# Kernel tuning notes

Measured on AMD Instinct MI355X. Metric: run time of the kernel, lower is better.

## Reference

```python
import jax, jax.numpy as jnp
import numpy as np

T, DIM, H = 1024, 2048, 16
QLR, KVLR = 1024, 512
NOPE, ROPE, VD = 128, 64, 128
QKD = NOPE + ROPE          # 192
IH, ID, TOPK = 16, 128, 256
EPS = 1e-6

def rmsnorm(x, w):
    return x * jax.lax.rsqrt(jnp.mean(x * x, axis=-1, keepdims=True) + EPS) * w

def layernorm(x, w, b, eps=1e-5):
    m = jnp.mean(x, axis=-1, keepdims=True)
    v = jnp.mean((x - m) ** 2, axis=-1, keepdims=True)
    return (x - m) * jax.lax.rsqrt(v + eps) * w + b

def apply_rope(x, cos, sin):
    # non-interleaved: first half = real, second half = imag
    d = x.shape[-1] // 2
    while cos.ndim < x.ndim:
        cos, sin = cos[:, None], sin[:, None]
    x1, x2 = x[..., :d], x[..., d:]
    return jnp.concatenate([x1 * cos - x2 * sin, x1 * sin + x2 * cos], axis=-1)

def hadamard(x):
    # unnormalized Walsh-Hadamard on last dim (power of 2)
    n = x.shape[-1]
    shape = x.shape
    y, h = x, 1
    while h < n:
        y = y.reshape(shape[:-1] + (-1, 2 * h))
        a, b = y[..., :h], y[..., h:]
        y = jnp.concatenate([a + b, a - b], axis=-1)
        h *= 2
    return y.reshape(shape)

def rotate_activation(x):
    # half-swap then Hadamard on each half
    d = x.shape[-1] // 2
    x1, x2 = x[..., :d], x[..., d:]
    return jnp.concatenate([hadamard(x2), hadamard(x1)], axis=-1)

def setup_inputs() -> dict:
    key = jax.random.key(0)
    ks = jax.random.split(key, 10)
    s = 0.02
    w = lambda k, shp: jax.random.normal(k, shp, jnp.float32) * s
    pos = jnp.arange(T, dtype=jnp.float32)
    inv = 1.0 / (10000.0 ** (jnp.arange(0, ROPE, 2, dtype=jnp.float32) / ROPE))
    ang = pos[:, None] * inv[None, :]
    return {
        'hidden_states': jax.random.normal(ks[0], (T, DIM), jnp.float32),
        'rope_cos': jnp.cos(ang), 'rope_sin': jnp.sin(ang),
        'wq_a': w(ks[1], (QLR, DIM)),
        'q_norm_w': jnp.ones((QLR,), jnp.float32),
        'wq_b': w(ks[2], (H * QKD, QLR)),
        'wkv_a': w(ks[3], (KVLR + ROPE, DIM)),
        'kv_norm_w': jnp.ones((KVLR,), jnp.float32),
        'wkv_b': w(ks[4], (H * (NOPE + VD), KVLR)),
        'wo': w(ks[5], (DIM, H * VD)),
        'iq_norm_w': jnp.ones((QLR,), jnp.float32),
        'iwq_b': w(ks[6], (IH * ID, QLR)),
        'iwk': w(ks[7], (IH * ID, DIM)),
        'k_norm_w': jnp.ones((ID,), jnp.float32),
        'k_norm_b': jnp.zeros((ID,), jnp.float32),
        'wproj': w(ks[8], (IH, DIM)),
    }

def reference(hidden_states, rope_cos, rope_sin, wq_a, q_norm_w, wq_b,
              wkv_a, kv_norm_w, wkv_b, wo, iq_norm_w, iwq_b, iwk,
              k_norm_w, k_norm_b, wproj):
    x = hidden_states
    t = x.shape[0]
    qr = x @ wq_a.T                                   # [t, QLR]

    # ---- lightning indexer: top-k causal token selection ----
    iq = (rmsnorm(qr, iq_norm_w) @ iwq_b.T).reshape(t, IH, ID)
    iq = jnp.concatenate([apply_rope(iq[..., :ROPE], rope_cos, rope_sin), iq[..., ROPE:]], -1)
    iq = rotate_activation(iq)
    ik = layernorm((x @ iwk.T).reshape(t, IH, ID), k_norm_w, k_norm_b)
    ik = jnp.concatenate([apply_rope(ik[..., :ROPE], rope_cos, rope_sin), ik[..., ROPE:]], -1)
    ik = rotate_activation(ik)
    w = (x @ wproj.T) * (IH ** -0.5) * (ID ** -0.5)   # [t, IH]
    dots = jax.nn.relu(jnp.einsum('thd,shd->ths', iq, ik)) * w[:, :, None]
    score = dots.sum(axis=1)                          # [t, t]
    rows = jnp.arange(t)
    score = jnp.where(rows[None, :] <= rows[:, None], score, -jnp.inf)
    _, topk_idx = jax.lax.top_k(score, TOPK)          # [t, TOPK]
    valid = topk_idx <= rows[:, None]
    safe_idx = jnp.where(valid, topk_idx, 0)

    # ---- MLA latent projections ----
    q = (rmsnorm(qr, q_norm_w) @ wq_b.T).reshape(t, H, QKD)
    q_nope, q_pe = q[..., :NOPE], q[..., NOPE:]
    q_pe = apply_rope(q_pe, rope_cos, rope_sin)
    kv_a = x @ wkv_a.T                                # [t, KVLR+ROPE]
    kv = rmsnorm(kv_a[:, :KVLR], kv_norm_w)
    k_pe = apply_rope(kv_a[:, KVLR:], rope_cos, rope_sin)
    wkv = wkv_b.reshape(H, NOPE + VD, KVLR)
    w_k, w_v = wkv[:, :NOPE, :], wkv[:, NOPE:, :]
    q_nope_proj = jnp.einsum('thd,hdc->thc', q_nope, w_k)
    q_key = jnp.concatenate([q_nope_proj, q_pe], -1)  # [t, H, KVLR+ROPE]
    kv_key = jnp.concatenate([kv, k_pe], -1)          # [t, KVLR+ROPE]

    # ---- sparse attention over selected indices ----
    sel = kv_key[safe_idx]                            # [t, TOPK, KVLR+ROPE]
    scale = QKD ** -0.5
    logits = jnp.einsum('thc,tkc->thk', q_key, sel) * scale
    logits = jnp.where(valid[:, None, :], logits, -jnp.inf)
    attn = jax.nn.softmax(logits, axis=-1)
    out_latent = jnp.einsum('thk,tkc->thc', attn, sel[..., :KVLR])
    out_v = jnp.einsum('thc,hdc->thd', out_latent, w_v)
    return out_v.reshape(t, H * VD) @ wo.T            # [t, DIM]
```

## Files before the change

### kernel.cpp

```cpp
#include <hip/hip_runtime.h>
#include <hip/hip_bf16.h>
#include <math.h>

#define T_     1024
#define DIM_   2048
#define H_     16
#define QLR_   1024
#define KVLR_  512
#define NOPE_  128
#define ROPE_  64
#define VD_    128
#define QKD_   192
#define IH_    16
#define ID_    128
#define TOPK_  256
#define CKV_   576

#define SCALE_W    0.022097086912079608f
#define SCALE_LOG  0.07216878364870323f

typedef short bfrag __attribute__((ext_vector_type(8)));
typedef float ffrag __attribute__((ext_vector_type(4)));

__device__ __forceinline__ unsigned short f2bf(float f) {
    union { __hip_bfloat16 h; unsigned short u; } c; c.h = __float2bfloat16(f); return c.u;
}
__device__ __forceinline__ float bf2f(unsigned short u) {
    union { unsigned short u; __hip_bfloat16 h; } c; c.u = u; return __bfloat162float(c.h);
}

__global__ __launch_bounds__(256) void cast_hl_k(
    const float* __restrict__ in, unsigned short* __restrict__ hi,
    unsigned short* __restrict__ lo, long n,
    const float* __restrict__ colw, const float* __restrict__ rowscale, int Kc)
{
    long base = ((long)blockIdx.x * 256 + threadIdx.x) * 4;
    if (base >= n) return;
    float4 v = *(const float4*)(in + base);
    float s[4] = {v.x, v.y, v.z, v.w};
    if (colw) {
        int col = (int)(base % Kc);
        float4 cw = *(const float4*)(colw + col);
        s[0] *= cw.x; s[1] *= cw.y; s[2] *= cw.z; s[3] *= cw.w;
    }
    if (rowscale) {
        float r = rowscale[base / Kc];
        s[0] *= r; s[1] *= r; s[2] *= r; s[3] *= r;
    }
    ushort4 h4;
    h4.x = f2bf(s[0]); h4.y = f2bf(s[1]); h4.z = f2bf(s[2]); h4.w = f2bf(s[3]);
    *(ushort4*)(hi + base) = h4;
    if (lo) {
        ushort4 l4;
        l4.x = f2bf(s[0] - bf2f(h4.x));
        l4.y = f2bf(s[1] - bf2f(h4.y));
        l4.z = f2bf(s[2] - bf2f(h4.z));
        l4.w = f2bf(s[3] - bf2f(h4.w));
        *(ushort4*)(lo + base) = l4;
    }
}

__global__ __launch_bounds__(256) void tcast_k(const float* __restrict__ in,
                                               unsigned short* __restrict__ out)
{
    int h = blockIdx.z, c0 = blockIdx.x * 32, d0 = blockIdx.y * 32;
    __shared__ float t[32][33];
    int tx = threadIdx.x & 31, ty = threadIdx.x >> 5;
    #pragma unroll
    for (int i = 0; i < 4; ++i)
        t[ty + i * 8][tx] = in[(long)(h * 256 + d0 + ty + i * 8) * 512 + c0 + tx];
    __syncthreads();
    #pragma unroll
    for (int i = 0; i < 4; ++i)
        out[((long)h * 512 + c0 + ty + i * 8) * 128 + d0 + tx] = f2bf(t[tx][ty + i * 8]);
}

__global__ __launch_bounds__(256) void gemm_bt_mfma_k(
    const unsigned short* __restrict__ A, const unsigned short* __restrict__ B,
    float* __restrict__ C, long sA, long sB, long sC,
    int lda, int ldb, int ldc, int N, int K)
{
    A += (long)blockIdx.z * sA;
    B += (long)blockIdx.z * sB;
    C += (long)blockIdx.z * sC;
    __shared__ unsigned short As[128 * 40];
    __shared__ unsigned short Bs[128 * 40];
    const int tid = threadIdx.x;
    const int bm = blockIdx.y * 128, bn = blockIdx.x * 128;
    const int wave = tid >> 6, lane = tid & 63;
    const int wm = (wave >> 1) * 64, wn = (wave & 1) * 64;
    const int lm = lane & 15, quad = lane >> 4;

    ffrag acc[4][4];
    #pragma unroll
    for (int mi = 0; mi < 4; ++mi)
        #pragma unroll
        for (int ni = 0; ni < 4; ++ni)
            #pragma unroll
            for (int r = 0; r < 4; ++r) acc[mi][ni][r] = 0.f;

    const int srow = tid >> 1, shalf = tid & 1;
    const long aoff = (long)(bm + srow) * lda + shalf * 16;
    int brow = bn + srow; if (brow > N - 1) brow = N - 1;
    const long boff = (long)brow * ldb + shalf * 16;
    unsigned short* la = As + srow * 40 + shalf * 16;
    unsigned short* lb = Bs + srow * 40 + shalf * 16;

    uint4 va0 = *(const uint4*)(A + aoff);
    uint4 va1 = *(const uint4*)(A + aoff + 8);
    uint4 vb0 = *(const uint4*)(B + boff);
    uint4 vb1 = *(const uint4*)(B + boff + 8);

    for (int k0 = 0; k0 < K; k0 += 32) {
        __syncthreads();
        *(uint4*)la = va0; *(uint4*)(la + 8) = va1;
        *(uint4*)lb = vb0; *(uint4*)(lb + 8) = vb1;
        __syncthreads();
        if (k0 + 32 < K) {
            va0 = *(const uint4*)(A + aoff + k0 + 32);
            va1 = *(const uint4*)(A + aoff + k0 + 40);
            vb0 = *(const uint4*)(B + boff + k0 + 32);
            vb1 = *(const uint4*)(B + boff + k0 + 40);
        }
        bfrag af[4], bf[4];
        #pragma unroll
        for (int mi = 0; mi < 4; ++mi)
            af[mi] = *(const bfrag*)(As + (wm + mi * 16 + lm) * 40 + quad * 8);
        #pragma unroll
        for (int ni = 0; ni < 4; ++ni)
            bf[ni] = *(const bfrag*)(Bs + (wn + ni * 16 + lm) * 40 + quad * 8);
        #pragma unroll
        for (int mi = 0; mi < 4; ++mi)
            #pragma unroll
            for (int ni = 0; ni < 4; ++ni)
                acc[mi][ni] = __builtin_amdgcn_mfma_f32_16x16x32_bf16(
                    af[mi], bf[ni], acc[mi][ni], 0, 0, 0);
    }

    #pragma unroll
    for (int mi = 0; mi < 4; ++mi)
        #pragma unroll
        for (int ni = 0; ni < 4; ++ni) {
            int n = bn + wn + ni * 16 + lm;
            if (n < N) {
                int mb = bm + wm + mi * 16 + quad * 4;
                #pragma unroll
                for (int r = 0; r < 4; ++r)
                    C[(long)(mb + r) * ldc + n] = acc[mi][ni][r];
            }
        }
}

__global__ __launch_bounds__(256) void gemm_bt64_k(
    const unsigned short* __restrict__ A, const unsigned short* __restrict__ B,
    void* __restrict__ Cv, long sA, long sB, long sC,
    int lda, int ldb, int ldc, int N, int K, int obf)
{
    A += (long)blockIdx.z * sA;
    B += (long)blockIdx.z * sB;
    __shared__ unsigned short As[64 * 40];
    __shared__ unsigned short Bs[64 * 40];
    const int tid = threadIdx.x;
    const int bm = blockIdx.y * 64, bn = blockIdx.x * 64;
    const int wave = tid >> 6, lane = tid & 63;
    const int wm = (wave >> 1) * 32, wn = (wave & 1) * 32;
    const int lm = lane & 15, quad = lane >> 4;

    ffrag acc[2][2];
    #pragma unroll
    for (int mi = 0; mi < 2; ++mi)
        #pragma unroll
        for (int ni = 0; ni < 2; ++ni)
            #pragma unroll
            for (int r = 0; r < 4; ++r) acc[mi][ni][r] = 0.f;

    const int srow = tid >> 2, schunk = tid & 3;
    const long aoff = (long)(bm + srow) * lda + schunk * 8;
    int brow = bn + srow; if (brow > N - 1) brow = N - 1;
    const long boff = (long)brow * ldb + schunk * 8;
    unsigned short* la = As + srow * 40 + schunk * 8;
    unsigned short* lb = Bs + srow * 40 + schunk * 8;

    uint4 va = *(const uint4*)(A + aoff);
    uint4 vb = *(const uint4*)(B + boff);

    for (int k0 = 0; k0 < K; k0 += 32) {
        __syncthreads();
        *(uint4*)la = va;
        *(uint4*)lb = vb;
        __syncthreads();
        if (k0 + 32 < K) {
            va = *(const uint4*)(A + aoff + k0 + 32);
            vb = *(const uint4*)(B + boff + k0 + 32);
        }
        bfrag af[2], bf[2];
        #pragma unroll
        for (int mi = 0; mi < 2; ++mi)
            af[mi] = *(const bfrag*)(As + (wm + mi * 16 + lm) * 40 + quad * 8);
        #pragma unroll
        for (int ni = 0; ni < 2; ++ni)
            bf[ni] = *(const bfrag*)(Bs + (wn + ni * 16 + lm) * 40 + quad * 8);
        #pragma unroll
        for (int mi = 0; mi < 2; ++mi)
            #pragma unroll
            for (int ni = 0; ni < 2; ++ni)
                acc[mi][ni] = __builtin_amdgcn_mfma_f32_16x16x32_bf16(
                    af[mi], bf[ni], acc[mi][ni], 0, 0, 0);
    }

    #pragma unroll
    for (int mi = 0; mi < 2; ++mi)
        #pragma unroll
        for (int ni = 0; ni < 2; ++ni) {
            int n = bn + wn + ni * 16 + lm;
            if (n < N) {
                int mb = bm + wm + mi * 16 + quad * 4;
                if (obf) {
                    unsigned short* C = (unsigned short*)Cv + (long)blockIdx.z * sC;
                    #pragma unroll
                    for (int r = 0; r < 4; ++r)
                        C[(long)(mb + r) * ldc + n] = f2bf(acc[mi][ni][r]);
                } else {
                    float* C = (float*)Cv + (long)blockIdx.z * sC;
                    #pragma unroll
                    for (int r = 0; r < 4; ++r)
                        C[(long)(mb + r) * ldc + n] = acc[mi][ni][r];
                }
            }
        }
}

// ... 11 lines not shown

    ffrag acc[2][2];
    #pragma unroll
    for (int mi = 0; mi < 2; ++mi)
        #pragma unroll
        for (int ni = 0; ni < 2; ++ni)
            #pragma unroll
            for (int r = 0; r < 4; ++r) acc[mi][ni][r] = 0.f;

    const int srow = tid >> 2, schunk = tid & 3;
    const long aoff = (long)(bm + srow) * lda + schunk * 8;
    const long boff = (long)(bn + srow) * ldb + schunk * 8;
    const int loff = srow * 40 + schunk * 8;

    uint4 vah = *(const uint4*)(Ah + aoff);
    uint4 val = *(const uint4*)(Al + aoff);
    uint4 vbh = *(const uint4*)(Bh + boff);
    uint4 vbl = *(const uint4*)(Bl + boff);

    for (int k0 = 0; k0 < K; k0 += 32) {
        __syncthreads();
        *(uint4*)(Ahs + loff) = vah;
        *(uint4*)(Als + loff) = val;
        *(uint4*)(Bhs + loff) = vbh;
        *(uint4*)(Bls + loff) = vbl;
        __syncthreads();
        if (k0 + 32 < K) {
            vah = *(const uint4*)(Ah + aoff + k0 + 32);
            val = *(const uint4*)(Al + aoff + k0 + 32);
            vbh = *(const uint4*)(Bh + boff + k0 + 32);
            vbl = *(const uint4*)(Bl + boff + k0 + 32);
        }
        bfrag ah[2], al[2], bh[2], bl[2];
        #pragma unroll
        for (int mi = 0; mi < 2; ++mi) {
            ah[mi] = *(const bfrag*)(Ahs + (wm + mi * 16 + lm) * 40 + quad * 8);
            al[mi] = *(const bfrag*)(Als + (wm + mi * 16 + lm) * 40 + quad * 8);
        }
        #pragma unroll
        for (int ni = 0; ni < 2; ++ni) {
            bh[ni] = *(const bfrag*)(Bhs + (wn + ni * 16 + lm) * 40 + quad * 8);
            bl[ni] = *(const bfrag*)(Bls + (wn + ni * 16 + lm) * 40 + quad * 8);
        }
        #pragma unroll
        for (int mi = 0; mi < 2; ++mi)
            #pragma unroll
            for (int ni = 0; ni < 2; ++ni) {
                acc[mi][ni] = __builtin_amdgcn_mfma_f32_16x16x32_bf16(ah[mi], bh[ni], acc[mi][ni], 0, 0, 0);
                acc[mi][ni] = __builtin_amdgcn_mfma_f32_16x16x32_bf16(ah[mi], bl[ni], acc[mi][ni], 0, 0, 0);
                acc[mi][ni] = __builtin_amdgcn_mfma_f32_16x16x32_bf16(al[mi], bh[ni], acc[mi][ni], 0, 0, 0);
            }
    }

    #pragma unroll
    for (int mi = 0; mi < 2; ++mi)
        #pragma unroll
        for (int ni = 0; ni < 2; ++ni) {
            int n = bn + wn + ni * 16 + lm;
            int mb = bm + wm + mi * 16 + quad * 4;
            #pragma unroll
            for (int r = 0; r < 4; ++r)
                C[(long)(mb + r) * ldc + n] = acc[mi][ni][r];
        }
}

__global__ __launch_bounds__(256) void wtok_k(const float* __restrict__ x,
    const float* __restrict__ wproj, float* __restrict__ wtok)
{
    int t = blockIdx.x, tid = threadIdx.x;
    __shared__ float xs[DIM_];
    for (int c = tid; c < DIM_; c += 256) xs[c] = x[(long)t * DIM_ + c];
    __syncthreads();
    int wave = tid >> 6, lane = tid & 63;
    #pragma unroll
    for (int i = 0; i < 4; ++i) {
        int h = wave * 4 + i;
        float s = 0.f;
        for (int c = lane; c < DIM_; c += 64) s += xs[c] * wproj[(long)h * DIM_ + c];
        for (int off = 32; off; off >>= 1) s += __shfl_xor(s, off, 64);
        if (lane == 0) wtok[(long)t * IH_ + h] = s * SCALE_W;
    }
}

__global__ __launch_bounds__(256) void rstd_k(const float* __restrict__ qr, float* __restrict__ rstd)
{
    int t = blockIdx.x, tid = threadIdx.x;
    float s = 0.f;
    for (int c = tid; c < QLR_; c += 256) { float v = qr[(long)t * QLR_ + c]; s += v * v; }
    __shared__ float red[256];
    red[tid] = s; __syncthreads();
    for (int off = 128; off; off >>= 1) { if (tid < off) red[tid] += red[tid + off]; __syncthreads(); }
    if (tid == 0) rstd[t] = rsqrtf(red[0] / (float)QLR_ + 1e-6f);
}

__device__ __forceinline__ void rope_rotate_128(float* s, float* w2, int tid, int t,
    const float* __restrict__ cosb, const float* __restrict__ sinb)
{
    float n1 = 0.f, n2 = 0.f;
    if (tid < 32) {
        float x1 = s[tid], x2 = s[tid + 32];
        float c = cosb[t * 32 + tid], sn = sinb[t * 32 + tid];
        n1 = x1 * c - x2 * sn;
        n2 = x1 * sn + x2 * c;
    }
    __syncthreads();
    if (tid < 32) { s[tid] = n1; s[tid + 32] = n2; }
    __syncthreads();
    const int g = tid >> 6, p = tid & 63;
    w2[tid] = s[((1 - g) << 6) + p];
    __syncthreads();
    #pragma unroll
    for (int h = 1; h < 64; h <<= 1) {
        float a = w2[tid], b = w2[(g << 6) + (p ^ h)];
        __syncthreads();
        w2[tid] = (p & h) ? (b - a) : (a + b);
        __syncthreads();
    }
}

__global__ __launch_bounds__(128) void transform_iq_k(float* __restrict__ iq,
    const float* __restrict__ cosb, const float* __restrict__ sinb)
{
    int row = blockIdx.x;
    int t = row / IH_;
    int tid = threadIdx.x;
    __shared__ float s[128], w2[128];
    s[tid] = iq[(long)row * 128 + tid];
    __syncthreads();
    rope_rotate_128(s, w2, tid, t, cosb, sinb);
    iq[(long)row * 128 + tid] = w2[tid];
}

__global__ __launch_bounds__(128) void transform_ik_k(float* __restrict__ ik,
    const float* __restrict__ knw, const float* __restrict__ knb,
    const float* __restrict__ cosb, const float* __restrict__ sinb)
{
    int row = blockIdx.x;
    int t = row / IH_;
    int tid = threadIdx.x;
    __shared__ float s[128], w2[128], red[128];
    float v = ik[(long)row * 128 + tid];
    red[tid] = v; __syncthreads();
    for (int off = 64; off; off >>= 1) { if (tid < off) red[tid] += red[tid + off]; __syncthreads(); }
    float m = red[0] / 128.f; __syncthreads();
    float d = v - m;
    red[tid] = d * d; __syncthreads();
    for (int off = 64; off; off >>= 1) { if (tid < off) red[tid] += red[tid + off]; __syncthreads(); }
    float var = red[0] / 128.f;
    s[tid] = d * rsqrtf(var + 1e-5f) * knw[tid] + knb[tid];
    __syncthreads();
    rope_rotate_128(s, w2, tid, t, cosb, sinb);
    ik[(long)row * 128 + tid] = w2[tid];
}

__global__ __launch_bounds__(256) void transform_kv_k(const float* __restrict__ kva,
    float* __restrict__ kvkey, const float* __restrict__ kvnw,
    const float* __restrict__ cosb, const float* __restrict__ sinb)
{
    int t = blockIdx.x, tid = threadIdx.x;
    const float* a = kva + (long)t * CKV_;
    float* o = kvkey + (long)t * CKV_;
    float v0 = a[tid], v1 = a[tid + 256];
    __shared__ float red[256];
    __shared__ float rsh;
    red[tid] = v0 * v0 + v1 * v1; __syncthreads();
    for (int off = 128; off; off >>= 1) { if (tid < off) red[tid] += red[tid + off]; __syncthreads(); }
    if (tid == 0) rsh = rsqrtf(red[0] / (float)KVLR_ + 1e-6f);
    __syncthreads();
    float rs = rsh;
    o[tid]       = v0 * rs * kvnw[tid];
    o[tid + 256] = v1 * rs * kvnw[tid + 256];
    if (tid < 32) {
        float x1 = a[512 + tid], x2 = a[544 + tid];
        float c = cosb[t * 32 + tid], sn = sinb[t * 32 + tid];
        o[512 + tid] = x1 * c - x2 * sn;
        o[544 + tid] = x1 * sn + x2 * c;
    }
}

__global__ __launch_bounds__(64) void qpe_k(const float* __restrict__ q, float* __restrict__ qkey,
    const float* __restrict__ cosb, const float* __restrict__ sinb)
{
    int row = blockIdx.x * 2 + (threadIdx.x >> 5);
    int i = threadIdx.x & 31;
    int t = row / H_;
    const float* qp = q + (long)row * QKD_ + NOPE_;
    float x1 = qp[i], x2 = qp[i + 32];
    float c = cosb[t * 32 + i], sn = sinb[t * 32 + i];
    float* o = qkey + (long)row * CKV_ + 512;
    o[i]      = x1 * c - x2 * sn;
    o[i + 32] = x1 * sn + x2 * c;
}

__global__ __launch_bounds__(256) void score3_k(
    const unsigned short* __restrict__ iqh, const unsigned short* __restrict__ iql,
    const unsigned short* __restrict__ ikh, const unsigned short* __restrict__ ikl,
    const float* __restrict__ wtok, float* __restrict__ score)
{
    const int bt = blockIdx.y, bs = blockIdx.x;
    if (bs > bt) return;
    __shared__ unsigned short Ah[64 * 40], Al[64 * 40], Bh[64 * 40], Bl[64 * 40];
    __shared__ float wts[64][16];
    const int tid = threadIdx.x;
    const int wave = tid >> 6, lane = tid & 63;
    const int wm = (wave >> 1) * 32, wn = (wave & 1) * 32;
    const int lm = lane & 15, quad = lane >> 4;
    const int t0 = bt * 64, s0 = bs * 64;
    const int srow = tid >> 2, schunk = tid & 3;
    const int loff = srow * 40 + schunk * 8;

    for (int e = tid; e < 1024; e += 256)
        wts[e >> 4][e & 15] = wtok[(long)(t0 + (e >> 4)) * IH_ + (e & 15)];

    const long abase = (long)(t0 + srow) * 2048 + schunk * 8;
    const long bbase = (long)(s0 + srow) * 2048 + schunk * 8;

    uint4 pah = *(const uint4*)(iqh + abase);
    uint4 pal = *(const uint4*)(iql + abase);
    uint4 pbh = *(const uint4*)(ikh + bbase);
    uint4 pbl = *(const uint4*)(ikl + bbase);

    float accf[2][2][4] = {};

    for (int h = 0; h < IH_; ++h) {
        ffrag acch[2][2];
        #pragma unroll
        for (int mi = 0; mi < 2; ++mi)
            #pragma unroll
            for (int ni = 0; ni < 2; ++ni)
                #pragma unroll
                for (int r = 0; r < 4; ++r) acch[mi][ni][r] = 0.f;

        #pragma unroll
        for (int k0 = 0; k0 < ID_; k0 += 32) {
            __syncthreads();
            *(uint4*)(Ah + loff) = pah;
            *(uint4*)(Al + loff) = pal;
            *(uint4*)(Bh + loff) = pbh;
            *(uint4*)(Bl + loff) = pbl;
            __syncthreads();
            int step = h * 4 + (k0 >> 5) + 1;
            if (step < 64) {
                int off = (step >> 2) * 128 + (step & 3) * 32;
                pah = *(const uint4*)(iqh + abase + off);
                pal = *(const uint4*)(iql + abase + off);
                pbh = *(const uint4*)(ikh + bbase + off);
                pbl = *(const uint4*)(ikl + bbase + off);
            }
            bfrag ahf[2], alf[2], bhf[2], blf[2];
            #pragma unroll
            for (int mi = 0; mi < 2; ++mi) {
                ahf[mi] = *(const bfrag*)(Ah + (wm + mi * 16 + lm) * 40 + quad * 8);
                alf[mi] = *(const bfrag*)(Al + (wm + mi * 16 + lm) * 40 + quad * 8);
            }
            #pragma unroll
            for (int ni = 0; ni < 2; ++ni) {
                bhf[ni] = *(const bfrag*)(Bh + (wn + ni * 16 + lm) * 40 + quad * 8);
                blf[ni] = *(const bfrag*)(Bl + (wn + ni * 16 + lm) * 40 + quad * 8);
            }
            #pragma unroll
            for (int mi = 0; mi < 2; ++mi)
                #pragma unroll
                for (int ni = 0; ni < 2; ++ni) {
                    acch[mi][ni] = __builtin_amdgcn_mfma_f32_16x16x32_bf16(ahf[mi], bhf[ni], acch[mi][ni], 0, 0, 0);
                    acch[mi][ni] = __builtin_amdgcn_mfma_f32_16x16x32_bf16(ahf[mi], blf[ni], acch[mi][ni], 0, 0, 0);
                    acch[mi][ni] = __builtin_amdgcn_mfma_f32_16x16x32_bf16(alf[mi], bhf[ni], acch[mi][ni], 0, 0, 0);
                }
        }
        #pragma unroll
        for (int mi = 0; mi < 2; ++mi) {
            float wr[4];
            #pragma unroll
            for (int r = 0; r < 4; ++r) wr[r] = wts[wm + mi * 16 + quad * 4 + r][h];
            #pragma unroll
            for (int ni = 0; ni < 2; ++ni)
                #pragma unroll
                for (int r = 0; r < 4; ++r)
                    accf[mi][ni][r] += fmaxf(acch[mi][ni][r], 0.f) * wr[r];
        }
    }
    #pragma unroll
    for (int mi = 0; mi < 2; ++mi)
        #pragma unroll
        for (int ni = 0; ni < 2; ++ni) {
            int s = s0 + wn + ni * 16 + lm;
            int tb = t0 + wm + mi * 16 + quad * 4;
            #pragma unroll
            for (int r = 0; r < 4; ++r)
                score[(long)(tb + r) * T_ + s] = accf[mi][ni][r];
        }
}

__global__ __launch_bounds__(512) void topk_k(const float* __restrict__ score, int* __restrict__ topk)
{
    int t = blockIdx.x, tid = threadIdx.x;
    __shared__ float v[1024];
    __shared__ int ix[1024];
    for (int i = tid; i < 1024; i += 512) {
        v[i] = (i <= t) ? score[(long)t * T_ + i] : -INFINITY;
        ix[i] = i;
    }
    __syncthreads();
    for (int k = 2; k <= 1024; k <<= 1) {
        for (int j = k >> 1; j > 0; j >>= 1) {
            for (int i = tid; i < 1024; i += 512) {
                int l = i ^ j;
                if (l > i) {
                    bool up = ((i & k) == 0);
                    float vi = v[i], vl = v[l];
                    int xi = ix[i], xl = ix[l];
                    bool iBetter = (vi > vl) || (vi == vl && xi < xl);
                    bool doSwap = up ? !iBetter : iBetter;
                    if (doSwap) { v[i] = vl; v[l] = vi; ix[i] = xl; ix[l] = xi; }
                }
            }
            __syncthreads();
        }
    }
    if (tid < 256) topk[(long)t * TOPK_ + tid] = ix[tid];
}

__global__ __launch_bounds__(256, 4) void attn3_k(
    const float* __restrict__ qkey, const unsigned short* __restrict__ kvb,
    const int* __restrict__ topkp, unsigned short* __restrict__ olat)
{
    __shared__ unsigned short U[13568];
    __shared__ float red[16 * 17];
    __shared__ int kidx[256];
    unsigned short* Qbf = U;
    float*          Lg  = (float*)U;
    unsigned short* VT0 = U;
    unsigned short* VT1 = U + 4608;
    unsigned short* Pbf = U + 9344;

    const int t = blockIdx.x, tid = threadIdx.x;
    const int wave = tid >> 6, lane = tid & 63;
    const int lm = lane & 15, quad = lane >> 4;

    kidx[tid] = topkp[(long)t * TOPK_ + tid];
    const float4* q4 = (const float4*)(qkey + (long)t * (H_ * CKV_));
    #pragma unroll
    for (int rep = 0; rep < 9; ++rep) {
        int e4 = rep * 256 + tid;
        float4 v = q4[e4];
        int f = e4 * 4, h = f / CKV_, c = f - h * CKV_;
        ushort4 u4; u4.x = f2bf(v.x); u4.y = f2bf(v.y); u4.z = f2bf(v.z); u4.w = f2bf(v.w);
        *(ushort4*)(Qbf + h * 584 + c) = u4;
    }
    int myk0 = topkp[(long)t * TOPK_ + wave * 64 + 0 * 16 + lm];
    int myk1 = topkp[(long)t * TOPK_ + wave * 64 + 1 * 16 + lm];
    int myk2 = topkp[(long)t * TOPK_ + wave * 64 + 2 * 16 + lm];
    int myk3 = topkp[(long)t * TOPK_ + wave * 64 + 3 * 16 + lm];
    __syncthreads();

    ffrag acc[4];
    #pragma unroll
    for (int ni = 0; ni < 4; ++ni)
        #pragma unroll
        for (int r = 0; r < 4; ++r) acc[ni][r] = 0.f;

    const unsigned short* kb0 = kvb + (long)myk0 * CKV_ + quad * 8;
    const unsigned short* kb1 = kvb + (long)myk1 * CKV_ + quad * 8;
    const unsigned short* kb2 = kvb + (long)myk2 * CKV_ + quad * 8;
    const unsigned short* kb3 = kvb + (long)myk3 * CKV_ + quad * 8;

    bfrag ba[4], bb[4], bc[4];
    #define LDT(DST, C) { \
        DST[0] = *(const bfrag*)(kb0 + (C)); \
        DST[1] = *(const bfrag*)(kb1 + (C)); \
        DST[2] = *(const bfrag*)(kb2 + (C)); \
        DST[3] = *(const bfrag*)(kb3 + (C)); }
    #define PHA_STEP(I, BUF) { \
        bfrag af = *(const bfrag*)(Qbf + lm * 584 + (I) * 32 + quad * 8); \
        _Pragma("unroll") \
        for (int ni = 0; ni < 4; ++ni) \
            acc[ni] = __builtin_amdgcn_mfma_f32_16x16x32_bf16(af, BUF[ni], acc[ni], 0, 0, 0); \
        if ((I) < 15) LDT(BUF, (I) * 32 + 96) }

    LDT(ba, 0) LDT(bb, 32) LDT(bc, 64)
    PHA_STEP(0, ba)  PHA_STEP(1, bb)  PHA_STEP(2, bc)
    PHA_STEP(3, ba)  PHA_STEP(4, bb)  PHA_STEP(5, bc)
    PHA_STEP(6, ba)  PHA_STEP(7, bb)  PHA_STEP(8, bc)
    PHA_STEP(9, ba)  PHA_STEP(10, bb) PHA_STEP(11, bc)
    PHA_STEP(12, ba) PHA_STEP(13, bb) PHA_STEP(14, bc)
    PHA_STEP(15, ba) PHA_STEP(16, bb) PHA_STEP(17, bc)
    #undef PHA_STEP
    #undef LDT

    __syncthreads();
    #pragma unroll
    for (int ni = 0; ni < 4; ++ni)
        #pragma unroll
        for (int r = 0; r < 4; ++r)
            Lg[(quad * 4 + r) * 260 + wave * 64 + ni * 16 + lm] = acc[ni][r];
    __syncthreads();

    {
        int h = tid >> 4, j = tid & 15;
        float m = -INFINITY;
        #pragma unroll
        for (int kk = 0; kk < 16; ++kk) {
            int key = j * 16 + kk;
            if (kidx[key] <= t) m = fmaxf(m, Lg[h * 260 + key]);
        }
        red[h * 17 + j] = m;
        __syncthreads();
        float mh = -INFINITY;
        #pragma unroll
        for (int jj = 0; jj < 16; ++jj) mh = fmaxf(mh, red[h * 17 + jj]);
        __syncthreads();
        float s = 0.f;
        float pv[16];
        #pragma unroll
        for (int kk = 0; kk < 16; ++kk) {
            int key = j * 16 + kk;
            float e = (kidx[key] <= t) ? expf(Lg[h * 260 + key] * SCALE_LOG - mh * SCALE_LOG) : 0.f;
            pv[kk] = e; s += e;
        }
        red[h * 17 + j] = s;
        __syncthreads();
        float sh = 0.f;
        #pragma unroll
        for (int jj = 0; jj < 16; ++jj) sh += red[h * 17 + jj];
        float inv = 1.f / sh;
        #pragma unroll
        for (int kk = 0; kk < 16; ++kk)
            Pbf[h * 264 + j * 16 + kk] = f2bf(pv[kk] * inv);
    }

    const int kpair = tid & 15, cgrp = tid >> 4;
// ... 8 lines not shown
        int ka_ = kidx[((IT) & 7) * 32 + 2 * kpair]; \
        int kb_ = kidx[((IT) & 7) * 32 + 2 * kpair + 1]; \
        long co_ = (long)(((IT) >> 3) * 128 + cgrp * 8); \
        GA = *(const uint4*)(kvb + (long)ka_ * CKV_ + co_); \
        GB = *(const uint4*)(kvb + (long)kb_ * CKV_ + co_); }
    #define STOREB(GA, GB, BUF) { \
        const unsigned short* pa_ = (const unsigned short*)&GA; \
        const unsigned short* pb_ = (const unsigned short*)&GB; \
        _Pragma("unroll") \
        for (int i_ = 0; i_ < 8; ++i_) \
            *(unsigned int*)((BUF) + (cgrp * 8 + i_) * 36 + 2 * kpair) = \
                (unsigned int)pa_[i_] | ((unsigned int)pb_[i_] << 16); }
    #define MFMAB(BUF, IT) { \
        bfrag pa = *(const bfrag*)(Pbf + lm * 264 + ((IT) & 7) * 32 + quad * 8); \
        _Pragma("unroll") \
        for (int ci = 0; ci < 2; ++ci) { \
            int c = wave * 32 + ci * 16 + lm; \
            bfrag bv; \
            ((uint2*)&bv)[0] = *(const uint2*)((BUF) + c * 36 + quad * 8); \
            ((uint2*)&bv)[1] = *(const uint2*)((BUF) + c * 36 + quad * 8 + 4); \
            acc2[ci] = __builtin_amdgcn_mfma_f32_16x16x32_bf16(pa, bv, acc2[ci], 0, 0, 0); } }
    #define OLATST(IT) { \
        int p_ = (IT) >> 3; \
        _Pragma("unroll") \
        for (int ci = 0; ci < 2; ++ci) \
            _Pragma("unroll") \
            for (int r = 0; r < 4; ++r) \
                olat[((long)t * H_ + quad * 4 + r) * 512 + p_ * 128 + wave * 32 + ci * 16 + lm] \
                    = f2bf(acc2[ci][r]); \
        _Pragma("unroll") \
        for (int ci = 0; ci < 2; ++ci) \
            _Pragma("unroll") \
            for (int r = 0; r < 4; ++r) acc2[ci][r] = 0.f; }
    #define LGKBAR() { asm volatile("s_waitcnt lgkmcnt(0)" ::: "memory"); \
                       __builtin_amdgcn_s_barrier(); }

    PREFB(ga0, gb0, 0);
    PREFB(ga1, gb1, 1);
    LGKBAR();
    STOREB(ga0, gb0, VT0);
    LGKBAR();
    for (int it = 0; it < 32; it += 2) {
        STOREB(ga1, gb1, VT1);
        MFMAB(VT0, it);
        if (it + 2 < 32) PREFB(ga0, gb0, it + 2);
        LGKBAR();
        if (it + 2 < 32) STOREB(ga0, gb0, VT0);
        MFMAB(VT1, it + 1);
        if (it + 3 < 32) PREFB(ga1, gb1, it + 3);
        if (((it + 1) & 7) == 7) OLATST(it + 1);
        LGKBAR();
    }
    #undef PREFB
    #undef STOREB
    #undef MFMAB
    #undef OLATST
    #undef LGKBAR
}

extern "C" void kernel_launch(void* const* d_in, const int* in_sizes, int n_in,
                              void* d_out, int out_size, void* d_ws, size_t ws_size,
                              hipStream_t stream)
{
    const float* x          = (const float*)d_in[0];
    const float* cosb       = (const float*)d_in[1];
    const float* sinb       = (const float*)d_in[2];
    const float* wq_a       = (const float*)d_in[3];
    const float* q_norm_w   = (const float*)d_in[4];
    const float* wq_b       = (const float*)d_in[5];
    const float* wkv_a      = (const float*)d_in[6];
    const float* kv_norm_w  = (const float*)d_in[7];
    const float* wkv_b      = (const float*)d_in[8];
    const float* wo         = (const float*)d_in[9];
    const float* iq_norm_w  = (const float*)d_in[10];
    const float* iwq_b      = (const float*)d_in[11];
    const float* iwk        = (const float*)d_in[12];
    const float* k_norm_w   = (const float*)d_in[13];
    const float* k_norm_b   = (const float*)d_in[14];
    const float* wproj      = (const float*)d_in[15];
    float* out = (float*)d_out;

    float* ws    = (float*)d_ws;
    float* qr    = ws;
    float* rstd  = ws + 1048576;
    float* wtok  = ws + 1049600;
    float* kvkey = ws + 1065984;
    int*   topk  = (int*)(ws + 1655808);
    float* qkey  = ws + 1917952;
    float* outv  = ws + 11355136;
    float* U0    = ws + 13452288;
    float* iq    = U0;
    float* ik    = U0 + 2097152;
    float* kva   = U0 + 4194304;
    float* qbuf  = U0 + 4784128;
    float* score = U0 + 7929856;

    unsigned short* qkey_u = (unsigned short*)qkey;
    unsigned short* wqa_hi  = qkey_u;
    unsigned short* wqa_lo  = qkey_u + 2097152;
    unsigned short* iwk_hi  = qkey_u + 4194304;
    unsigned short* iwk_lo  = qkey_u + 8388608;
    unsigned short* iwqb_hi = qkey_u + 12582912;
    unsigned short* iwqb_lo = qkey_u + 14680064;
    unsigned short* qriq_hi = qkey_u + 16777216;
    unsigned short* qriq_lo = qkey_u + 17825792;
    unsigned short* iqbf_hi = qkey_u;
    unsigned short* iqbf_lo = qkey_u + 2097152;
    unsigned short* ikbf_hi = qkey_u + 4194304;
    unsigned short* ikbf_lo = qkey_u + 6291456;
    unsigned short* wkvb_bf = qkey_u + 8388608;
    unsigned short* wo_bf   = qkey_u + 12582912;
    unsigned short* q_u     = (unsigned short*)qbuf;
    unsigned short* x_hi    = q_u;
    unsigned short* x_lo    = q_u + 2097152;
    unsigned short* wkva_hi = q_u + 4194304;
    unsigned short* outv_u  = (unsigned short*)outv;
    unsigned short* wqb_hi  = outv_u;
    unsigned short* qrq_hi  = outv_u + 3145728;
    unsigned short* outv_bf = outv_u;
    unsigned short* qbf     = (unsigned short*)iq;
    unsigned short* wkT     = (unsigned short*)ik;
    unsigned short* kvb     = (unsigned short*)qr;
    unsigned short* olat_bf = (unsigned short*)U0;

    #define CAST(src, hi, lo, n, cw, rs, K) \
        cast_hl_k<<<(n)/1024, 256, 0, stream>>>((src), (hi), (lo), (n), (cw), (rs), (K))

    CAST(x,     x_hi,   x_lo,   2097152L, nullptr, nullptr, 0);
    CAST(wq_a,  wqa_hi, wqa_lo, 2097152L, nullptr, nullptr, 0);
    CAST(iwk,   iwk_hi, iwk_lo, 4194304L, nullptr, nullptr, 0);
    CAST(iwq_b, iwqb_hi,iwqb_lo,2097152L, nullptr, nullptr, 0);
    CAST(wkv_a, wkva_hi,nullptr,1179648L, nullptr, nullptr, 0);
    CAST(wq_b,  wqb_hi, nullptr,3145728L, nullptr, nullptr, 0);

    gemm3_bt64_k<<<dim3(QLR_/64, T_/64), 256, 0, stream>>>(
        x_hi, x_lo, wqa_hi, wqa_lo, qr, DIM_, DIM_, QLR_, DIM_);

    rstd_k<<<T_, 256, 0, stream>>>(qr, rstd);
    CAST(qr, qriq_hi, qriq_lo, 1048576L, iq_norm_w, rstd, QLR_);
    CAST(qr, qrq_hi,  nullptr, 1048576L, q_norm_w,  rstd, QLR_);

    gemm3_bt64_k<<<dim3(IH_*ID_/64, T_/64), 256, 0, stream>>>(
        qriq_hi, qriq_lo, iwqb_hi, iwqb_lo, iq, QLR_, QLR_, IH_*ID_, QLR_);
    gemm3_bt64_k<<<dim3(IH_*ID_/64, T_/64), 256, 0, stream>>>(
        x_hi, x_lo, iwk_hi, iwk_lo, ik, DIM_, DIM_, IH_*ID_, DIM_);

    gemm_bt64_k<<<dim3((CKV_+63)/64, T_/64, 1), 256, 0, stream>>>(
        x_hi, wkva_hi, kva, 0,0,0, DIM_, DIM_, CKV_, CKV_, DIM_, 0);

    gemm_bt64_k<<<dim3(H_*QKD_/64, T_/64, 1), 256, 0, stream>>>(
        qrq_hi, wqb_hi, qbuf, 0,0,0, QLR_, QLR_, H_*QKD_, H_*QKD_, QLR_, 0);

    wtok_k<<<T_, 256, 0, stream>>>(x, wproj, wtok);

    transform_iq_k<<<T_*IH_, 128, 0, stream>>>(iq, cosb, sinb);
    transform_ik_k<<<T_*IH_, 128, 0, stream>>>(ik, k_norm_w, k_norm_b, cosb, sinb);
    transform_kv_k<<<T_, 256, 0, stream>>>(kva, kvkey, kv_norm_w, cosb, sinb);

    CAST(kvkey, kvb, nullptr, 589824L, nullptr, nullptr, 0);

    CAST(iq, iqbf_hi, iqbf_lo, 2097152L, nullptr, nullptr, 0);
    CAST(ik, ikbf_hi, ikbf_lo, 2097152L, nullptr, nullptr, 0);
    score3_k<<<dim3(T_/64, T_/64), 256, 0, stream>>>(iqbf_hi, iqbf_lo, ikbf_hi, ikbf_lo, wtok, score);
    topk_k<<<T_, 512, 0, stream>>>(score, topk);

    CAST(qbuf, qbf, nullptr, 3145728L, nullptr, nullptr, 0);
    tcast_k<<<dim3(16, 4, 16), 256, 0, stream>>>(wkv_b, wkT);
    qpe_k<<<T_*H_/2, 64, 0, stream>>>(qbuf, qkey, cosb, sinb);
    gemm_bt_mfma_k<<<dim3(KVLR_/128, T_/128, H_), 256, 0, stream>>>(
        qbf, wkT, qkey, 192L, 65536L, 576L, H_*QKD_, ID_, H_*CKV_, KVLR_, ID_);

    attn3_k<<<T_, 256, 0, stream>>>(qkey, kvb, topk, olat_bf);

    CAST(wkv_b, wkvb_bf, nullptr, 2097152L, nullptr, nullptr, 0);
    gemm_bt64_k<<<dim3(VD_/64, T_/64, H_), 256, 0, stream>>>(
        olat_bf, wkvb_bf + (long)NOPE_*KVLR_, outv_bf,
        512L, (long)(NOPE_+VD_)*KVLR_, (long)VD_,
        H_*KVLR_, KVLR_, H_*VD_, VD_, KVLR_, 1);

    CAST(wo, wo_bf, nullptr, 4194304L, nullptr, nullptr, 0);
    gemm_bt64_k<<<dim3(DIM_/64, T_/64, 1), 256, 0, stream>>>(
        outv_bf, wo_bf, out, 0,0,0, H_*VD_, H_*VD_, DIM_, DIM_, H_*VD_, 0);

    #undef CAST
    (void)in_sizes; (void)n_in; (void)out_size; (void)ws_size;
}
```

Baseline: 596.0 us.

## Fuse casts and norm/rope transforms, emit bf16 directly, batch weight casts

Merges the six upfront fp32-to-bf16 casts and the two late weight casts into multi-segment cast launches. Fuses the q rmsnorm statistics with both normalized casts, and rewrites the iq/ik/kv transforms with wave-shuffle Hadamard that write bf16 hi/lo outputs directly. The qkey GEMM and qpe now write bf16, so attention loads bf16 queries without converting. This removes several launches and fp32 round trips through memory. It also changes workspace buffer offsets, which risks aliasing between buffers.

```diff
diff --git a/kernel.cpp b/kernel.cpp
--- a/kernel.cpp
+++ b/kernel.cpp
@@ -31,33 +31,81 @@
 
 __global__ __launch_bounds__(256) void cast_hl_k(
     const float* __restrict__ in, unsigned short* __restrict__ hi,
-    unsigned short* __restrict__ lo, long n,
-    const float* __restrict__ colw, const float* __restrict__ rowscale, int Kc)
+    unsigned short* __restrict__ lo, long n)
 {
     long base = ((long)blockIdx.x * 256 + threadIdx.x) * 4;
     if (base >= n) return;
     float4 v = *(const float4*)(in + base);
-    float s[4] = {v.x, v.y, v.z, v.w};
-    if (colw) {
-        int col = (int)(base % Kc);
-        float4 cw = *(const float4*)(colw + col);
-        s[0] *= cw.x; s[1] *= cw.y; s[2] *= cw.z; s[3] *= cw.w;
-    }
-    if (rowscale) {
-        float r = rowscale[base / Kc];
-        s[0] *= r; s[1] *= r; s[2] *= r; s[3] *= r;
-    }
     ushort4 h4;
-    h4.x = f2bf(s[0]); h4.y = f2bf(s[1]); h4.z = f2bf(s[2]); h4.w = f2bf(s[3]);
+    h4.x = f2bf(v.x); h4.y = f2bf(v.y); h4.z = f2bf(v.z); h4.w = f2bf(v.w);
     *(ushort4*)(hi + base) = h4;
     if (lo) {
         ushort4 l4;
-        l4.x = f2bf(s[0] - bf2f(h4.x));
-        l4.y = f2bf(s[1] - bf2f(h4.y));
-        l4.z = f2bf(s[2] - bf2f(h4.z));
-        l4.w = f2bf(s[3] - bf2f(h4.w));
+        l4.x = f2bf(v.x - bf2f(h4.x));
+        l4.y = f2bf(v.y - bf2f(h4.y));
+        l4.z = f2bf(v.z - bf2f(h4.z));
+        l4.w = f2bf(v.w - bf2f(h4.w));
         *(ushort4*)(lo + base) = l4;
     }
+}
+
+struct CastSeg { const float* src; unsigned short* hi; unsigned short* lo; };
+struct CastDesc { CastSeg seg[6]; int bstart[7]; int nseg; };
+
+__global__ __launch_bounds__(256) void castm_k(CastDesc d)
+{
+    int b = blockIdx.x, s = 0;
+    #pragma unroll
+    for (int i = 1; i < 6; ++i) if (i < d.nseg && b >= d.bstart[i]) s = i;
+    long base = ((long)(b - d.bstart[s]) * 256 + threadIdx.x) * 4;
+    float4 v = *(const float4*)(d.seg[s].src + base);
+    ushort4 h4;
+    h4.x = f2bf(v.x); h4.y = f2bf(v.y); h4.z = f2bf(v.z); h4.w = f2bf(v.w);
+    *(ushort4*)(d.seg[s].hi + base) = h4;
+    if (d.seg[s].lo) {
+        ushort4 l4;
+        l4.x = f2bf(v.x - bf2f(h4.x));
+        l4.y = f2bf(v.y - bf2f(h4.y));
+        l4.z = f2bf(v.z - bf2f(h4.z));
+        l4.w = f2bf(v.w - bf2f(h4.w));
+        *(ushort4*)(d.seg[s].lo + base) = l4;
+    }
+}
+
+__global__ __launch_bounds__(256) void qrnorm_k(const float* __restrict__ qr,
+    const float* __restrict__ iqw, const float* __restrict__ qw,
+    unsigned short* __restrict__ qriq_hi, unsigned short* __restrict__ qriq_lo,
+    unsigned short* __restrict__ qrq_hi)
+{
+    int t = blockIdx.x, tid = threadIdx.x;
+    long base = (long)t * QLR_ + tid * 4;
+    float4 v = *(const float4*)(qr + base);
+    __shared__ float red[256];
+    red[tid] = v.x * v.x + v.y * v.y + v.z * v.z + v.w * v.w;
+    __syncthreads();
+    for (int off = 128; off; off >>= 1) { if (tid < off) red[tid] += red[tid + off]; __syncthreads(); }
+    float r = rsqrtf(red[0] / (float)QLR_ + 1e-6f);
+    int col = tid * 4;
+    float4 wi = *(const float4*)(iqw + col);
+    float4 wq = *(const float4*)(qw + col);
+    float s[4] = {v.x, v.y, v.z, v.w};
+    float wiv[4] = {wi.x, wi.y, wi.z, wi.w};
+    float wqv[4] = {wq.x, wq.y, wq.z, wq.w};
+    ushort4 h4, l4, g4;
+    unsigned short* hp = (unsigned short*)&h4;
+    unsigned short* lp = (unsigned short*)&l4;
+    unsigned short* gp = (unsigned short*)&g4;
+    #pragma unroll
+    for (int i = 0; i < 4; ++i) {
+        float ai = s[i] * wiv[i] * r;
+        float aq = s[i] * wqv[i] * r;
+        hp[i] = f2bf(ai);
+        lp[i] = f2bf(ai - bf2f(hp[i]));
+        gp[i] = f2bf(aq);
+    }
+    *(ushort4*)(qriq_hi + base) = h4;
+    *(ushort4*)(qriq_lo + base) = l4;
+    *(ushort4*)(qrq_hi + base) = g4;
 }
 
 __global__ __launch_bounds__(256) void tcast_k(const float* __restrict__ in,
@@ -77,12 +125,11 @@
 
 __global__ __launch_bounds__(256) void gemm_bt_mfma_k(
     const unsigned short* __restrict__ A, const unsigned short* __restrict__ B,
-    float* __restrict__ C, long sA, long sB, long sC,
-    int lda, int ldb, int ldc, int N, int K)
+    void* __restrict__ Cv, long sA, long sB, long sC,
+    int lda, int ldb, int ldc, int N, int K, int obf)
 {
     A += (long)blockIdx.z * sA;
     B += (long)blockIdx.z * sB;
-    C += (long)blockIdx.z * sC;
     __shared__ unsigned short As[128 * 40];
     __shared__ unsigned short Bs[128 * 40];
     const int tid = threadIdx.x;
@@ -144,9 +191,17 @@
             int n = bn + wn + ni * 16 + lm;
             if (n < N) {
                 int mb = bm + wm + mi * 16 + quad * 4;
-                #pragma unroll
-                for (int r = 0; r < 4; ++r)
-                    C[(long)(mb + r) * ldc + n] = acc[mi][ni][r];
+                if (obf) {
+                    unsigned short* C = (unsigned short*)Cv + (long)blockIdx.z * sC;
+                    #pragma unroll
+                    for (int r = 0; r < 4; ++r)
+                        C[(long)(mb + r) * ldc + n] = f2bf(acc[mi][ni][r]);
+                } else {
+                    float* C = (float*)Cv + (long)blockIdx.z * sC;
+                    #pragma unroll
+                    for (int r = 0; r < 4; ++r)
+                        C[(long)(mb + r) * ldc + n] = acc[mi][ni][r];
+                }
             }
         }
 }
@@ -324,84 +379,77 @@
     }
 }
 
-__global__ __launch_bounds__(256) void rstd_k(const float* __restrict__ qr, float* __restrict__ rstd)
-{
-    int t = blockIdx.x, tid = threadIdx.x;
-    float s = 0.f;
-    for (int c = tid; c < QLR_; c += 256) { float v = qr[(long)t * QLR_ + c]; s += v * v; }
-    __shared__ float red[256];
-    red[tid] = s; __syncthreads();
-    for (int off = 128; off; off >>= 1) { if (tid < off) red[tid] += red[tid + off]; __syncthreads(); }
-    if (tid == 0) rstd[t] = rsqrtf(red[0] / (float)QLR_ + 1e-6f);
-}
-
-__device__ __forceinline__ void rope_rotate_128(float* s, float* w2, int tid, int t,
+__global__ __launch_bounds__(256) void transform_iq2_k(const float* __restrict__ iq,
+    unsigned short* __restrict__ hi, unsigned short* __restrict__ lo,
     const float* __restrict__ cosb, const float* __restrict__ sinb)
 {
-    float n1 = 0.f, n2 = 0.f;
-    if (tid < 32) {
-        float x1 = s[tid], x2 = s[tid + 32];
-        float c = cosb[t * 32 + tid], sn = sinb[t * 32 + tid];
-        n1 = x1 * c - x2 * sn;
-        n2 = x1 * sn + x2 * c;
-    }
-    __syncthreads();
-    if (tid < 32) { s[tid] = n1; s[tid + 32] = n2; }
-    __syncthreads();
-    const int g = tid >> 6, p = tid & 63;
-    w2[tid] = s[((1 - g) << 6) + p];
-    __syncthreads();
+    int row = blockIdx.x * 4 + (threadIdx.x >> 6);
+    int p = threadIdx.x & 63;
+    int t = row >> 4;
+    float a = iq[(long)row * 128 + p];
+    float b = iq[(long)row * 128 + 64 + p];
+    float c = cosb[t * 32 + (p & 31)], sn = sinb[t * 32 + (p & 31)];
+    float asw = __shfl_xor(a, 32, 64);
+    a = (p < 32) ? (a * c - asw * sn) : (asw * sn + a * c);
     #pragma unroll
     for (int h = 1; h < 64; h <<= 1) {
-        float a = w2[tid], b = w2[(g << 6) + (p ^ h)];
-        __syncthreads();
-        w2[tid] = (p & h) ? (b - a) : (a + b);
-        __syncthreads();
-    }
-}
-
-__global__ __launch_bounds__(128) void transform_iq_k(float* __restrict__ iq,
-    const float* __restrict__ cosb, const float* __restrict__ sinb)
-{
-    int row = blockIdx.x;
-    int t = row / IH_;
-    int tid = threadIdx.x;
-    __shared__ float s[128], w2[128];
-    s[tid] = iq[(long)row * 128 + tid];
-    __syncthreads();
-    rope_rotate_128(s, w2, tid, t, cosb, sinb);
-    iq[(long)row * 128 + tid] = w2[tid];
-}
-
-__global__ __launch_bounds__(128) void transform_ik_k(float* __restrict__ ik,
+        float a2 = __shfl_xor(a, h, 64);
+        float b2 = __shfl_xor(b, h, 64);
+        a = (p & h) ? (a2 - a) : (a + a2);
+        b = (p & h) ? (b2 - b) : (b + b2);
+    }
+    unsigned short hb = f2bf(b), ha = f2bf(a);
+    hi[(long)row * 128 + p] = hb;
+    hi[(long)row * 128 + 64 + p] = ha;
+    lo[(long)row * 128 + p] = f2bf(b - bf2f(hb));
+    lo[(long)row * 128 + 64 + p] = f2bf(a - bf2f(ha));
+}
+
+__global__ __launch_bounds__(256) void transform_ik2_k(const float* __restrict__ ik,
+    unsigned short* __restrict__ hi, unsigned short* __restrict__ lo,
     const float* __restrict__ knw, const float* __restrict__ knb,
     const float* __restrict__ cosb, const float* __restrict__ sinb)
 {
-    int row = blockIdx.x;
-    int t = row / IH_;
-    int tid = threadIdx.x;
-    __shared__ float s[128], w2[128], red[128];
-    float v = ik[(long)row * 128 + tid];
-    red[tid] = v; __syncthreads();
-    for (int off = 64; off; off >>= 1) { if (tid < off) red[tid] += red[tid + off]; __syncthreads(); }
-    float m = red[0] / 128.f; __syncthreads();
-    float d = v - m;
-    red[tid] = d * d; __syncthreads();
-    for (int off = 64; off; off >>= 1) { if (tid < off) red[tid] += red[tid + off]; __syncthreads(); }
-    float var = red[0] / 128.f;
-    s[tid] = d * rsqrtf(var + 1e-5f) * knw[tid] + knb[tid];
-    __syncthreads();
-    rope_rotate_128(s, w2, tid, t, cosb, sinb);
-    ik[(long)row * 128 + tid] = w2[tid];
-}
-
-__global__ __launch_bounds__(256) void transform_kv_k(const float* __restrict__ kva,
-    float* __restrict__ kvkey, const float* __restrict__ kvnw,
+    int row = blockIdx.x * 4 + (threadIdx.x >> 6);
+    int p = threadIdx.x & 63;
+    int t = row >> 4;
+    float a = ik[(long)row * 128 + p];
+    float b = ik[(long)row * 128 + 64 + p];
+    float s = a + b;
+    #pragma unroll
+    for (int o = 1; o < 64; o <<= 1) s += __shfl_xor(s, o, 64);
+    float m = s * (1.f / 128.f);
+    float da = a - m, db = b - m;
+    float v = da * da + db * db;
+    #pragma unroll
+    for (int o = 1; o < 64; o <<= 1) v += __shfl_xor(v, o, 64);
+    float r = rsqrtf(v * (1.f / 128.f) + 1e-5f);
+    a = da * r * knw[p] + knb[p];
+    b = db * r * knw[64 + p] + knb[64 + p];
+    float c = cosb[t * 32 + (p & 31)], sn = sinb[t * 32 + (p & 31)];
+    float asw = __shfl_xor(a, 32, 64);
+    a = (p < 32) ? (a * c - asw * sn) : (asw * sn + a * c);
+    #pragma unroll
+    for (int h = 1; h < 64; h <<= 1) {
+        float a2 = __shfl_xor(a, h, 64);
+        float b2 = __shfl_xor(b, h, 64);
+        a = (p & h) ? (a2 - a) : (a + a2);
+        b = (p & h) ? (b2 - b) : (b + b2);
+    }
+    unsigned short hb = f2bf(b), ha = f2bf(a);
+    hi[(long)row * 128 + p] = hb;
+    hi[(long)row * 128 + 64 + p] = ha;
+    lo[(long)row * 128 + p] = f2bf(b - bf2f(hb));
+    lo[(long)row * 128 + 64 + p] = f2bf(a - bf2f(ha));
+}
+
+__global__ __launch_bounds__(256) void transform_kv2_k(const float* __restrict__ kva,
+    unsigned short* __restrict__ kvb, const float* __restrict__ kvnw,
     const float* __restrict__ cosb, const float* __restrict__ sinb)
 {
     int t = blockIdx.x, tid = threadIdx.x;
     const float* a = kva + (long)t * CKV_;
-    float* o = kvkey + (long)t * CKV_;
+    unsigned short* o = kvb + (long)t * CKV_;
     float v0 = a[tid], v1 = a[tid + 256];
     __shared__ float red[256];
     __shared__ float rsh;
@@ -410,17 +458,18 @@
     if (tid == 0) rsh = rsqrtf(red[0] / (float)KVLR_ + 1e-6f);
     __syncthreads();
     float rs = rsh;
-    o[tid]       = v0 * rs * kvnw[tid];
-    o[tid + 256] = v1 * rs * kvnw[tid + 256];
+    o[tid]       = f2bf(v0 * rs * kvnw[tid]);
+    o[tid + 256] = f2bf(v1 * rs * kvnw[tid + 256]);
     if (tid < 32) {
         float x1 = a[512 + tid], x2 = a[544 + tid];
         float c = cosb[t * 32 + tid], sn = sinb[t * 32 + tid];
-        o[512 + tid] = x1 * c - x2 * sn;
-        o[544 + tid] = x1 * sn + x2 * c;
-    }
-}
-
-__global__ __launch_bounds__(64) void qpe_k(const float* __restrict__ q, float* __restrict__ qkey,
+        o[512 + tid] = f2bf(x1 * c - x2 * sn);
+        o[544 + tid] = f2bf(x1 * sn + x2 * c);
+    }
+}
+
+__global__ __launch_bounds__(64) void qpe_k(const float* __restrict__ q,
+    unsigned short* __restrict__ qkeyb,
     const float* __restrict__ cosb, const float* __restrict__ sinb)
 {
     int row = blockIdx.x * 2 + (threadIdx.x >> 5);
@@ -429,9 +478,9 @@
     const float* qp = q + (long)row * QKD_ + NOPE_;
     float x1 = qp[i], x2 = qp[i + 32];
     float c = cosb[t * 32 + i], sn = sinb[t * 32 + i];
-    float* o = qkey + (long)row * CKV_ + 512;
-    o[i]      = x1 * c - x2 * sn;
-    o[i + 32] = x1 * sn + x2 * c;
+    unsigned short* o = qkeyb + (long)row * CKV_ + 512;
+    o[i]      = f2bf(x1 * c - x2 * sn);
+    o[i + 32] = f2bf(x1 * sn + x2 * c);
 }
 
 __global__ __launch_bounds__(256) void score3_k(
@@ -563,10 +612,10 @@
 }
 
 __global__ __launch_bounds__(256, 4) void attn3_k(
-    const float* __restrict__ qkey, const unsigned short* __restrict__ kvb,
+    const unsigned short* __restrict__ qkeyb, const unsigned short* __restrict__ kvb,
     const int* __restrict__ topkp, unsigned short* __restrict__ olat)
 {
-    __shared__ unsigned short U[13568];
+    __shared__ __align__(16) unsigned short U[13568];
     __shared__ float red[16 * 17];
     __shared__ int kidx[256];
     unsigned short* Qbf = U;
@@ -580,14 +629,13 @@
     const int lm = lane & 15, quad = lane >> 4;
 
     kidx[tid] = topkp[(long)t * TOPK_ + tid];
-    const float4* q4 = (const float4*)(qkey + (long)t * (H_ * CKV_));
+    const uint2* q2 = (const uint2*)(qkeyb + (long)t * (H_ * CKV_));
     #pragma unroll
     for (int rep = 0; rep < 9; ++rep) {
-        int e4 = rep * 256 + tid;
-        float4 v = q4[e4];
-        int f = e4 * 4, h = f / CKV_, c = f - h * CKV_;
-        ushort4 u4; u4.x = f2bf(v.x); u4.y = f2bf(v.y); u4.z = f2bf(v.z); u4.w = f2bf(v.w);
-        *(ushort4*)(Qbf + h * 584 + c) = u4;
+        int e = rep * 256 + tid;
+        uint2 v = q2[e];
+        int f = e * 4, h = f / CKV_, c = f - h * CKV_;
+        *(uint2*)(Qbf + h * 584 + c) = v;
     }
     int myk0 = topkp[(long)t * TOPK_ + wave * 64 + 0 * 16 + lm];
     int myk1 = topkp[(long)t * TOPK_ + wave * 64 + 1 * 16 + lm];
@@ -762,9 +810,7 @@
 
     float* ws    = (float*)d_ws;
     float* qr    = ws;
-    float* rstd  = ws + 1048576;
     float* wtok  = ws + 1049600;
-    float* kvkey = ws + 1065984;
     int*   topk  = (int*)(ws + 1655808);
     float* qkey  = ws + 1917952;
     float* outv  = ws + 11355136;
@@ -788,8 +834,9 @@
     unsigned short* iqbf_lo = qkey_u + 2097152;
     unsigned short* ikbf_hi = qkey_u + 4194304;
     unsigned short* ikbf_lo = qkey_u + 6291456;
-    unsigned short* wkvb_bf = qkey_u + 8388608;
-    unsigned short* wo_bf   = qkey_u + 12582912;
+    unsigned short* qkey_bf = qkey_u;
+    unsigned short* wkvb_bf = qkey_u + 9437184;
+    unsigned short* wo_bf   = qkey_u + 11534336;
     unsigned short* q_u     = (unsigned short*)qbuf;
     unsigned short* x_hi    = q_u;
     unsigned short* x_lo    = q_u + 2097152;
@@ -803,22 +850,24 @@
     unsigned short* kvb     = (unsigned short*)qr;
     unsigned short* olat_bf = (unsigned short*)U0;
 
-    #define CAST(src, hi, lo, n, cw, rs, K) \
-        cast_hl_k<<<(n)/1024, 256, 0, stream>>>((src), (hi), (lo), (n), (cw), (rs), (K))
-
-    CAST(x,     x_hi,   x_lo,   2097152L, nullptr, nullptr, 0);
-    CAST(wq_a,  wqa_hi, wqa_lo, 2097152L, nullptr, nullptr, 0);
-    CAST(iwk,   iwk_hi, iwk_lo, 4194304L, nullptr, nullptr, 0);
-    CAST(iwq_b, iwqb_hi,iwqb_lo,2097152L, nullptr, nullptr, 0);
-    CAST(wkv_a, wkva_hi,nullptr,1179648L, nullptr, nullptr, 0);
-    CAST(wq_b,  wqb_hi, nullptr,3145728L, nullptr, nullptr, 0);
+    {
+        CastDesc d;
+        d.seg[0] = { x,      x_hi,    x_lo    };
+        d.seg[1] = { wq_a,   wqa_hi,  wqa_lo  };
+        d.seg[2] = { iwk,    iwk_hi,  iwk_lo  };
+        d.seg[3] = { iwq_b,  iwqb_hi, iwqb_lo };
+        d.seg[4] = { wkv_a,  wkva_hi, nullptr };
+        d.seg[5] = { wq_b,   wqb_hi,  nullptr };
+        d.bstart[0] = 0;     d.bstart[1] = 2048;  d.bstart[2] = 4096;
+        d.bstart[3] = 8192;  d.bstart[4] = 10240; d.bstart[5] = 11392;
+        d.bstart[6] = 14464; d.nseg = 6;
+        castm_k<<<14464, 256, 0, stream>>>(d);
+    }
 
     gemm3_bt64_k<<<dim3(QLR_/64, T_/64), 256, 0, stream>>>(
         x_hi, x_lo, wqa_hi, wqa_lo, qr, DIM_, DIM_, QLR_, DIM_);
 
-    rstd_k<<<T_, 256, 0, stream>>>(qr, rstd);
-    CAST(qr, qriq_hi, qriq_lo, 1048576L, iq_norm_w, rstd, QLR_);
-    CAST(qr, qrq_hi,  nullptr, 1048576L, q_norm_w,  rstd, QLR_);
+    qrnorm_k<<<T_, 256, 0, stream>>>(qr, iq_norm_w, q_norm_w, qriq_hi, qriq_lo, qrq_hi);
 
     gemm3_bt64_k<<<dim3(IH_*ID_/64, T_/64), 256, 0, stream>>>(
         qriq_hi, qriq_lo, iwqb_hi, iwqb_lo, iq, QLR_, QLR_, IH_*ID_, QLR_);
@@ -833,35 +882,39 @@
 
     wtok_k<<<T_, 256, 0, stream>>>(x, wproj, wtok);
 
-    transform_iq_k<<<T_*IH_, 128, 0, stream>>>(iq, cosb, sinb);
-    transform_ik_k<<<T_*IH_, 128, 0, stream>>>(ik, k_norm_w, k_norm_b, cosb, sinb);
-    transform_kv_k<<<T_, 256, 0, stream>>>(kva, kvkey, kv_norm_w, cosb, sinb);
-
-    CAST(kvkey, kvb, nullptr, 589824L, nullptr, nullptr, 0);
-
-    CAST(iq, iqbf_hi, iqbf_lo, 2097152L, nullptr, nullptr, 0);
-    CAST(ik, ikbf_hi, ikbf_lo, 2097152L, nullptr, nullptr, 0);
+    transform_iq2_k<<<T_*IH_/4, 256, 0, stream>>>(iq, iqbf_hi, iqbf_lo, cosb, sinb);
+    transform_ik2_k<<<T_*IH_/4, 256, 0, stream>>>(ik, ikbf_hi, ikbf_lo, k_norm_w, k_norm_b, cosb, sinb);
+    transform_kv2_k<<<T_, 256, 0, stream>>>(kva, kvb, kv_norm_w, cosb, sinb);
+
     score3_k<<<dim3(T_/64, T_/64), 256, 0, stream>>>(iqbf_hi, iqbf_lo, ikbf_hi, ikbf_lo, wtok, score);
     topk_k<<<T_, 512, 0, stream>>>(score, topk);
 
-    CAST(qbuf, qbf, nullptr, 3145728L, nullptr, nullptr, 0);
+    cast_hl_k<<<3072, 256, 0, stream>>>(qbuf, qbf, nullptr, 3145728L);
     tcast_k<<<dim3(16, 4, 16), 256, 0, stream>>>(wkv_b, wkT);
-    qpe_k<<<T_*H_/2, 64, 0, stream>>>(qbuf, qkey, cosb, sinb);
+    qpe_k<<<T_*H_/2, 64, 0, stream>>>(qbuf, qkey_bf, cosb, sinb);
     gemm_bt_mfma_k<<<dim3(KVLR_/128, T_/128, H_), 256, 0, stream>>>(
-        qbf, wkT, qkey, 192L, 65536L, 576L, H_*QKD_, ID_, H_*CKV_, KVLR_, ID_);
-
-    attn3_k<<<T_, 256, 0, stream>>>(qkey, kvb, topk, olat_bf);
-
-    CAST(wkv_b, wkvb_bf, nullptr, 2097152L, nullptr, nullptr, 0);
+        qbf, wkT, qkey_bf, 192L, 65536L, 576L, H_*QKD_, ID_, H_*CKV_, KVLR_, ID_, 1);
+
+    attn3_k<<<T_, 256, 0, stream>>>(qkey_bf, kvb, topk, olat_bf);
+
+    {
+        CastDesc d;
+        d.seg[0] = { wkv_b, wkvb_bf, nullptr };
+        d.seg[1] = { wo,    wo_bf,   nullptr };
+        d.seg[2] = d.seg[0]; d.seg[3] = d.seg[0]; d.seg[4] = d.seg[0]; d.seg[5] = d.seg[0];
+        d.bstart[0] = 0; d.bstart[1] = 2048; d.bstart[2] = 6144;
+        d.bstart[3] = 6144; d.bstart[4] = 6144; d.bstart[5] = 6144; d.bstart[6] = 6144;
+        d.nseg = 2;
+        castm_k<<<6144, 256, 0, stream>>>(d);
+    }
+
     gemm_bt64_k<<<dim3(VD_/64, T_/64, H_), 256, 0, stream>>>(
         olat_bf, wkvb_bf + (long)NOPE_*KVLR_, outv_bf,
         512L, (long)(NOPE_+VD_)*KVLR_, (long)VD_,
         H_*KVLR_, KVLR_, H_*VD_, VD_, KVLR_, 1);
 
-    CAST(wo, wo_bf, nullptr, 4194304L, nullptr, nullptr, 0);
     gemm_bt64_k<<<dim3(DIM_/64, T_/64, 1), 256, 0, stream>>>(
         outv_bf, wo_bf, out, 0,0,0, H_*VD_, H_*VD_, DIM_, DIM_, H_*VD_, 0);
 
-    #undef CAST
     (void)in_sizes; (void)n_in; (void)out_size; (void)ws_size;
 }
```

Result: faster. 557.4 us (-6.5%).
